# Kernel tuning notes

Measured on AMD Instinct MI355X. Metric: run time of the kernel, lower is better.

## Reference

```python
import jax, jax.numpy as jnp
import numpy as np

EPS = 1e-6
THRESHOLD = 0.5


def ternarize(weight):
    # absmax scale along last dim (in_features)
    scale = jnp.clip(jnp.max(jnp.abs(weight), axis=-1, keepdims=True), EPS, None)
    normalized = weight / scale
    ternary = jnp.where(normalized > THRESHOLD, 1.0,
                        jnp.where(normalized < -THRESHOLD, -1.0, 0.0)).astype(weight.dtype)
    return ternary * scale


def setup_inputs() -> dict:
    key = jax.random.key(0)
    k1, k2, k3 = jax.random.split(key, 3)
    B, S, D_in, D_out = 4, 4096, 2048, 2048
    x = jax.random.normal(k1, (B, S, D_in), dtype=jnp.float32)
    # kaiming-uniform-ish init
    bound_w = (6.0 / D_in) ** 0.5 / (1.0 + 5.0) ** 0.5
    weight = jax.random.uniform(k2, (D_out, D_in), dtype=jnp.float32, minval=-bound_w, maxval=bound_w)
    bound_b = 1.0 / D_in ** 0.5
    bias = jax.random.uniform(k3, (D_out,), dtype=jnp.float32, minval=-bound_b, maxval=bound_b)
    return {"x": x, "weight": weight, "bias": bias}


def reference(x, weight, bias):
    qw = ternarize(weight)  # [out, in]
    # F.linear: x @ qw.T + bias
    return jnp.einsum('bsi,oi->bso', x, qw) + bias
```

## Files before the change

kernel.cpp:

```cpp
#include <hip/hip_runtime.h>
#include <hip/hip_bf16.h>
#include <stdint.h>


#define M_DIM 16384
#define N_DIM 2048
#define K_DIM 2048

#define BM 128
#define BN 128
#define BK 32

typedef __bf16 bf16x8 __attribute__((ext_vector_type(8)));
typedef float f32x4 __attribute__((ext_vector_type(4)));

__global__ __launch_bounds__(256) void cvt_x_k(
    const float* __restrict__ x, __hip_bfloat16* __restrict__ xb) {
  const size_t i = ((size_t)blockIdx.x * 256 + threadIdx.x) * 8;
  const float4 a = *(const float4*)(x + i);
  const float4 b = *(const float4*)(x + i + 4);
  bf16x8 o;
  o[0] = (__bf16)a.x; o[1] = (__bf16)a.y; o[2] = (__bf16)a.z; o[3] = (__bf16)a.w;
  o[4] = (__bf16)b.x; o[5] = (__bf16)b.y; o[6] = (__bf16)b.z; o[7] = (__bf16)b.w;
  *(bf16x8*)((__bf16*)xb + i) = o;
}

__global__ __launch_bounds__(256) void ternarize_k(
    const float* __restrict__ w,
    __hip_bfloat16* __restrict__ qw,
    float* __restrict__ scales) {
  const int row = blockIdx.x;
  const float* wr = w + (size_t)row * K_DIM;

  float m = 0.0f;
  for (int k = threadIdx.x; k < K_DIM; k += 256)
    m = fmaxf(m, fabsf(wr[k]));

  for (int off = 32; off > 0; off >>= 1)
    m = fmaxf(m, __shfl_down(m, off, 64));
  __shared__ float wmax[4];
  if ((threadIdx.x & 63) == 0) wmax[threadIdx.x >> 6] = m;
  __syncthreads();
  float scale = fmaxf(fmaxf(wmax[0], wmax[1]), fmaxf(wmax[2], wmax[3]));
  scale = fmaxf(scale, 1e-6f);
  if (threadIdx.x == 0) scales[row] = scale;

  for (int k = threadIdx.x; k < K_DIM; k += 256) {
    const float v = wr[k] / scale;
    const float t = (v > 0.5f) ? 1.0f : ((v < -0.5f) ? -1.0f : 0.0f);
    qw[(size_t)row * K_DIM + k] = __float2bfloat16(t);
  }
}

static __device__ __forceinline__ void async_cp16(const __hip_bfloat16* g,
                                                  __hip_bfloat16* l) {
  __builtin_amdgcn_global_load_lds(
      (__attribute__((address_space(1))) void*)const_cast<__hip_bfloat16*>(g),
      (__attribute__((address_space(3))) void*)(l), 16, 0, 0);
}

__global__ __launch_bounds__(256) void gemm_bt_k(
    const __hip_bfloat16* __restrict__ A,
    const __hip_bfloat16* __restrict__ B,
    const float* __restrict__ scales,
    const float* __restrict__ bias,
    float* __restrict__ C) {
  __shared__ __hip_bfloat16 As[BM * BK];
  __shared__ __hip_bfloat16 Bs[BN * BK];

  const int tid = threadIdx.x;
  const int wave = tid >> 6;
  const int lane = tid & 63;
  const int quad = lane >> 4;
  const int lrow = lane & 15;
  const int wm = wave >> 1;
  const int wn = wave & 1;

  const int m0 = blockIdx.y * BM;
  const int n0 = blockIdx.x * BN;

  const int c = tid;
  const __hip_bfloat16* Ag0 = A + (size_t)(m0 + (c >> 2)) * K_DIM + (c & 3) * 8;
  const __hip_bfloat16* Ag1 = A + (size_t)(m0 + ((c + 256) >> 2)) * K_DIM + (c & 3) * 8;
  const __hip_bfloat16* Bg0 = B + (size_t)(n0 + (c >> 2)) * K_DIM + (c & 3) * 8;
  const __hip_bfloat16* Bg1 = B + (size_t)(n0 + ((c + 256) >> 2)) * K_DIM + (c & 3) * 8;

  __hip_bfloat16* As_w0 = As + wave * 512;
  __hip_bfloat16* As_w1 = As + wave * 512 + 2048;
  __hip_bfloat16* Bs_w0 = Bs + wave * 512;
  __hip_bfloat16* Bs_w1 = Bs + wave * 512 + 2048;

  f32x4 acc[4][4] = {};

  for (int kk = 0; kk < K_DIM; kk += BK) {
    __syncthreads();
    async_cp16(Ag0 + kk, As_w0);
    async_cp16(Ag1 + kk, As_w1);
    async_cp16(Bg0 + kk, Bs_w0);
    async_cp16(Bg1 + kk, Bs_w1);
    __syncthreads();

    bf16x8 af[4], bfr[4];
    #pragma unroll
    for (int i = 0; i < 4; ++i)
      af[i] = *(const bf16x8*)(As + (wm * 64 + i * 16 + lrow) * BK + quad * 8);
    #pragma unroll
    for (int i = 0; i < 4; ++i)
      bfr[i] = *(const bf16x8*)(Bs + (wn * 64 + i * 16 + lrow) * BK + quad * 8);

    #pragma unroll
    for (int i = 0; i < 4; ++i)
      #pragma unroll
      for (int j = 0; j < 4; ++j)
        acc[i][j] = __builtin_amdgcn_mfma_f32_16x16x32_bf16(af[i], bfr[j], acc[i][j], 0, 0, 0);
  }

  #pragma unroll
  for (int j = 0; j < 4; ++j) {
    const int col = n0 + wn * 64 + j * 16 + lrow;
    const float s = scales[col];
    const float b = bias[col];
    #pragma unroll
    for (int i = 0; i < 4; ++i) {
      const int rbase = m0 + wm * 64 + i * 16 + quad * 4;
      #pragma unroll
      for (int r = 0; r < 4; ++r)
        C[(size_t)(rbase + r) * N_DIM + col] = acc[i][j][r] * s + b;
    }
  }
}

extern "C" void kernel_launch(void* const* d_in, const int* in_sizes, int n_in,
                              void* d_out, int out_size, void* d_ws, size_t ws_size,
                              hipStream_t stream) {
  const float* x    = (const float*)d_in[0];
  const float* w    = (const float*)d_in[1];
  const float* bias = (const float*)d_in[2];
  float* out = (float*)d_out;

  __hip_bfloat16* xb = (__hip_bfloat16*)d_ws;
  __hip_bfloat16* qw = (__hip_bfloat16*)((char*)d_ws + (size_t)M_DIM * K_DIM * 2);
  float* scales = (float*)((char*)d_ws + (size_t)M_DIM * K_DIM * 2 + (size_t)N_DIM * K_DIM * 2);

  cvt_x_k<<<dim3((M_DIM * (size_t)K_DIM) / (256 * 8)), dim3(256), 0, stream>>>(x, xb);
  ternarize_k<<<dim3(N_DIM), dim3(256), 0, stream>>>(w, qw, scales);
  gemm_bt_k<<<dim3(N_DIM / BN, M_DIM / BM), dim3(256), 0, stream>>>(xb, qw, scales, bias, out);
}
```

Before: 397.1 us.

## Fuse fp32-to-bf16 conversion of x into GEMM loads with XOR-swizzled LDS

Drops the separate x conversion kernel and the bf16 copy of x in workspace. The GEMM now streams fp32 x straight into LDS via async global-to-LDS copies and converts to bf16 when it loads fragments. It also adds XOR swizzling to both the A and B LDS layouts to reduce bank conflicts. The trade-off is twice the global and LDS traffic for A inside the GEMM, since each A tile is read 16 times across N blocks, plus conversion ALU work in the inner loop.

Measured after the change: 450.4 us. 13.4% more time.

```diff
diff --git a/kernel.cpp b/kernel.cpp
--- a/kernel.cpp
+++ b/kernel.cpp
@@ -13,17 +13,6 @@
 
 typedef __bf16 bf16x8 __attribute__((ext_vector_type(8)));
 typedef float f32x4 __attribute__((ext_vector_type(4)));
-
-__global__ __launch_bounds__(256) void cvt_x_k(
-    const float* __restrict__ x, __hip_bfloat16* __restrict__ xb) {
-  const size_t i = ((size_t)blockIdx.x * 256 + threadIdx.x) * 8;
-  const float4 a = *(const float4*)(x + i);
-  const float4 b = *(const float4*)(x + i + 4);
-  bf16x8 o;
-  o[0] = (__bf16)a.x; o[1] = (__bf16)a.y; o[2] = (__bf16)a.z; o[3] = (__bf16)a.w;
-  o[4] = (__bf16)b.x; o[5] = (__bf16)b.y; o[6] = (__bf16)b.z; o[7] = (__bf16)b.w;
-  *(bf16x8*)((__bf16*)xb + i) = o;
-}
 
 __global__ __launch_bounds__(256) void ternarize_k(
     const float* __restrict__ w,
@@ -52,20 +41,19 @@
   }
 }
 
-static __device__ __forceinline__ void async_cp16(const __hip_bfloat16* g,
-                                                  __hip_bfloat16* l) {
+static __device__ __forceinline__ void async_cp16(const void* g, void* l) {
   __builtin_amdgcn_global_load_lds(
-      (__attribute__((address_space(1))) void*)const_cast<__hip_bfloat16*>(g),
+      (__attribute__((address_space(1))) void*)const_cast<void*>(g),
       (__attribute__((address_space(3))) void*)(l), 16, 0, 0);
 }
 
 __global__ __launch_bounds__(256) void gemm_bt_k(
-    const __hip_bfloat16* __restrict__ A,
+    const float* __restrict__ A,
     const __hip_bfloat16* __restrict__ B,
     const float* __restrict__ scales,
     const float* __restrict__ bias,
     float* __restrict__ C) {
-  __shared__ __hip_bfloat16 As[BM * BK];
+  __shared__ float Asf[BM * BK];
   __shared__ __hip_bfloat16 Bs[BN * BK];
 
   const int tid = threadIdx.x;
@@ -79,34 +67,58 @@
   const int m0 = blockIdx.y * BM;
   const int n0 = blockIdx.x * BN;
 
-  const int c = tid;
-  const __hip_bfloat16* Ag0 = A + (size_t)(m0 + (c >> 2)) * K_DIM + (c & 3) * 8;
-  const __hip_bfloat16* Ag1 = A + (size_t)(m0 + ((c + 256) >> 2)) * K_DIM + (c & 3) * 8;
-  const __hip_bfloat16* Bg0 = B + (size_t)(n0 + (c >> 2)) * K_DIM + (c & 3) * 8;
-  const __hip_bfloat16* Bg1 = B + (size_t)(n0 + ((c + 256) >> 2)) * K_DIM + (c & 3) * 8;
+  const float* AgP[4];
+  float* AsP[4];
+  #pragma unroll
+  for (int s = 0; s < 4; ++s) {
+    const int L = tid + 256 * s;
+    const int r = L >> 3;
+    const int c = (L & 7) ^ (r & 7);
+    AgP[s] = A + (size_t)(m0 + r) * K_DIM + c * 4;
+    AsP[s] = Asf + (size_t)L * 4;
+  }
+  const __hip_bfloat16* BgP[2];
+  __hip_bfloat16* BsP[2];
+  #pragma unroll
+  for (int s = 0; s < 2; ++s) {
+    const int L = tid + 256 * s;
+    const int r = L >> 2;
+    const int c = (L & 3) ^ ((r >> 1) & 3);
+    BgP[s] = B + (size_t)(n0 + r) * K_DIM + c * 8;
+    BsP[s] = Bs + (size_t)L * 8;
+  }
 
-  __hip_bfloat16* As_w0 = As + wave * 512;
-  __hip_bfloat16* As_w1 = As + wave * 512 + 2048;
-  __hip_bfloat16* Bs_w0 = Bs + wave * 512;
-  __hip_bfloat16* Bs_w1 = Bs + wave * 512 + 2048;
+  const int sA = lrow & 7;
+  const int iloA = (2 * quad) ^ sA;
+  const int ihiA = iloA ^ 1;
+  const int cB = ((quad ^ ((lrow >> 1) & 3))) * 8;
 
   f32x4 acc[4][4] = {};
 
   for (int kk = 0; kk < K_DIM; kk += BK) {
     __syncthreads();
-    async_cp16(Ag0 + kk, As_w0);
-    async_cp16(Ag1 + kk, As_w1);
-    async_cp16(Bg0 + kk, Bs_w0);
-    async_cp16(Bg1 + kk, Bs_w1);
+    #pragma unroll
+    for (int s = 0; s < 4; ++s) async_cp16(AgP[s] + kk, AsP[s]);
+    #pragma unroll
+    for (int s = 0; s < 2; ++s) async_cp16(BgP[s] + kk, BsP[s]);
     __syncthreads();
 
     bf16x8 af[4], bfr[4];
     #pragma unroll
-    for (int i = 0; i < 4; ++i)
-      af[i] = *(const bf16x8*)(As + (wm * 64 + i * 16 + lrow) * BK + quad * 8);
+    for (int i = 0; i < 4; ++i) {
+      const float* rowb = Asf + (wm * 64 + i * 16 + lrow) * BK;
+      const f32x4 lo = *(const f32x4*)(rowb + iloA * 4);
+      const f32x4 hi = *(const f32x4*)(rowb + ihiA * 4);
+      bf16x8 f;
+      f[0] = (__bf16)lo[0]; f[1] = (__bf16)lo[1];
+      f[2] = (__bf16)lo[2]; f[3] = (__bf16)lo[3];
+      f[4] = (__bf16)hi[0]; f[5] = (__bf16)hi[1];
+      f[6] = (__bf16)hi[2]; f[7] = (__bf16)hi[3];
+      af[i] = f;
+    }
     #pragma unroll
     for (int i = 0; i < 4; ++i)
-      bfr[i] = *(const bf16x8*)(Bs + (wn * 64 + i * 16 + lrow) * BK + quad * 8);
+      bfr[i] = *(const bf16x8*)(Bs + (wn * 64 + i * 16 + lrow) * BK + cB);
 
     #pragma unroll
     for (int i = 0; i < 4; ++i)
@@ -138,11 +150,9 @@
   const float* bias = (const float*)d_in[2];
   float* out = (float*)d_out;
 
-  __hip_bfloat16* xb = (__hip_bfloat16*)d_ws;
-  __hip_bfloat16* qw = (__hip_bfloat16*)((char*)d_ws + (size_t)M_DIM * K_DIM * 2);
-  float* scales = (float*)((char*)d_ws + (size_t)M_DIM * K_DIM * 2 + (size_t)N_DIM * K_DIM * 2);
+  __hip_bfloat16* qw = (__hip_bfloat16*)d_ws;
+  float* scales = (float*)((char*)d_ws + (size_t)N_DIM * K_DIM * 2);
 
-  cvt_x_k<<<dim3((M_DIM * (size_t)K_DIM) / (256 * 8)), dim3(256), 0, stream>>>(x, xb);
   ternarize_k<<<dim3(N_DIM), dim3(256), 0, stream>>>(w, qw, scales);
-  gemm_bt_k<<<dim3(N_DIM / BN, M_DIM / BM), dim3(256), 0, stream>>>(xb, qw, scales, bias, out);
+  gemm_bt_k<<<dim3(N_DIM / BN, M_DIM / BM), dim3(256), 0, stream>>>(x, qw, scales, bias, out);
 }
```
